# Kernel tuning notes

Measured on AMD Instinct MI355X. Metric: run time of the kernel, lower is better.

Reference implementation:

```python
import jax, jax.numpy as jnp
import numpy as np

N, T, E, H, V = 32768, 20, 50, 50, 200
PAD = 0

def setup_inputs() -> dict:
    key = jax.random.key(0)
    ks = jax.random.split(key, 11)
    s = 1.0 / np.sqrt(H)  # torch LSTM init scale
    return {
        "char_indices": jax.random.randint(ks[0], (N, T), 0, V, dtype=jnp.int32),
        "word_lengths": jax.random.randint(ks[1], (N,), 0, T + 1, dtype=jnp.int32),
        "emb": jax.random.normal(ks[2], (V, E), jnp.float32) * 0.1,
        "W_ih_f": jax.random.normal(ks[3], (4 * H, E), jnp.float32) * s,
        "W_hh_f": jax.random.normal(ks[4], (4 * H, H), jnp.float32) * s,
        "b_ih_f": jax.random.normal(ks[5], (4 * H,), jnp.float32) * s,
        "b_hh_f": jax.random.normal(ks[6], (4 * H,), jnp.float32) * s,
        "W_ih_b": jax.random.normal(ks[7], (4 * H, E), jnp.float32) * s,
        "W_hh_b": jax.random.normal(ks[8], (4 * H, H), jnp.float32) * s,
        "b_ih_b": jax.random.normal(ks[9], (4 * H,), jnp.float32) * s,
        "b_hh_b": jax.random.normal(ks[10], (4 * H,), jnp.float32) * s,
    }

def _run_dir(x, lengths, W_ih, W_hh, b_ih, b_hh, reverse):
    # x: [N,T,E]; returns final hidden state [N,H] at the word's true boundary.
    n = x.shape[0]
    xg = jnp.einsum('nte,ge->ntg', x, W_ih) + b_ih + b_hh  # [N,T,4H]
    def step(carry, t):
        h, c = carry
        g = xg[:, t] + h @ W_hh.T  # [N,4H]
        i, f, gg, o = jnp.split(g, 4, axis=-1)
        c_new = jax.nn.sigmoid(f) * c + jax.nn.sigmoid(i) * jnp.tanh(gg)
        h_new = jax.nn.sigmoid(o) * jnp.tanh(c_new)
        valid = (t < lengths)[:, None]  # only update inside the word
        return (jnp.where(valid, h_new, h), jnp.where(valid, c_new, c)), None
    ts = jnp.arange(T - 1, -1, -1) if reverse else jnp.arange(T)
    z = jnp.zeros((n, W_hh.shape[1]), x.dtype)
    (h, _), _ = jax.lax.scan(step, (z, z), ts)
    return h

def reference(char_indices, word_lengths, emb, W_ih_f, W_hh_f, b_ih_f, b_hh_f,
              W_ih_b, W_hh_b, b_ih_b, b_hh_b):
    emb = emb.at[PAD].set(0.0)  # padding_idx row is zero
    x = emb[char_indices]  # [N,T,E]
    h_f = _run_dir(x, word_lengths, W_ih_f, W_hh_f, b_ih_f, b_hh_f, reverse=False)
    h_b = _run_dir(x, word_lengths, W_ih_b, W_hh_b, b_ih_b, b_hh_b, reverse=True)
    return jnp.concatenate([h_f, h_b], axis=-1)  # [N, 2H]
```

## Files before the change

### kernel.cpp

```cpp
#include <hip/hip_runtime.h>


#define TT    20
#define HH    50
#define VV    200
#define TILES 13
#define GSTR  212
#define GSH   (VV * GSTR)
#define WSH   (TILES * 16 * 64)
#define NW    32768
#define NB_G  50
#define NB_W  104
#define NB_H  128
#define NBLK  1024

#define N2LOG2E (-1.4426950408889634f)
#define P2LOG2E 2.8853900817779268f

typedef __attribute__((ext_vector_type(8))) short bf16x8;
typedef __attribute__((ext_vector_type(4))) float f32x4;

__device__ __forceinline__ float frcp(float x) { return __builtin_amdgcn_rcpf(x); }
#if __has_builtin(__builtin_amdgcn_exp2f)
__device__ __forceinline__ float fexp2(float x) { return __builtin_amdgcn_exp2f(x); }
#else
__device__ __forceinline__ float fexp2(float x) { return exp2f(x); }
#endif

__device__ __forceinline__ short f2bf(float x) {
    unsigned b = __builtin_bit_cast(unsigned, x);
    unsigned r = (b + 0x7FFFu + ((b >> 16) & 1u)) >> 16;
    return (short)r;
}
__device__ __forceinline__ float bfhi(unsigned w) {
    return __builtin_bit_cast(float, w & 0xFFFF0000u);
}
__device__ __forceinline__ float bflo(unsigned w) {
    return __builtin_bit_cast(float, w << 16);
}

__global__ void k_prep(const float* __restrict__ emb,
                       const float* __restrict__ Wih_f, const float* __restrict__ bih_f,
                       const float* __restrict__ bhh_f,
                       const float* __restrict__ Wih_b, const float* __restrict__ bih_b,
                       const float* __restrict__ bhh_b,
                       const float* __restrict__ Whh_f, const float* __restrict__ Whh_b,
                       const int* __restrict__ lens,
                       short* __restrict__ Gimg, short* __restrict__ Wimg,
                       int* __restrict__ cnt) {
    int blk = blockIdx.x;
    int tid = threadIdx.x;
    __shared__ float Wl[4 * HH * HH];
    __shared__ float bs[4 * HH];

    if (blk < NB_G) {
        int d = blk / 25;
        int vbase = (blk % 25) * 8;
        const float* Wih = d ? Wih_b : Wih_f;
        const float* bih = d ? bih_b : bih_f;
        const float* bhh = d ? bhh_b : bhh_f;
        for (int i = tid; i < 4 * HH * HH; i += 256) {
            int r = i / HH;
            float sc = (r / HH == 2) ? P2LOG2E : N2LOG2E;
            Wl[i] = Wih[i] * sc;
        }
        if (tid < 4 * HH) {
            float sc = (tid / HH == 2) ? P2LOG2E : N2LOG2E;
            bs[tid] = (bih[tid] + bhh[tid]) * sc;
        }
        __syncthreads();
        int r = tid;
        if (r < 4 * HH) {
            int g = r / HH, u = r % HH;
            #pragma unroll
            for (int vv = 0; vv < 8; ++vv) {
                int v = vbase + vv;
                float s = bs[r];
                if (v != 0) {
                    #pragma unroll 10
                    for (int e = 0; e < HH; ++e)
                        s = fmaf(emb[v * HH + e], Wl[r * HH + e], s);
                }
                Gimg[d * GSH + v * GSTR + u * 4 + g] = f2bf(s);
            }
        } else {
            for (int k = r - 4 * HH; k < 8 * 12; k += 56) {
                int v = vbase + k / 12;
                Gimg[d * GSH + v * GSTR + 4 * HH + (k % 12)] = 0;
            }
        }
    } else if (blk < NB_G + NB_W) {
        int idx = (blk - NB_G) * 256 + tid;
        if (idx >= 2 * WSH) return;
        int d = idx / WSH;
        int e = idx % WSH;
        int t = e >> 10, m = (e >> 6) & 15, k = e & 63;
        int u = 4 * t + (m >> 2), g = m & 3;
        const float* Whh = d ? Whh_b : Whh_f;
        float sc = (g == 2) ? P2LOG2E : N2LOG2E;
        float val = (k < HH && u < HH) ? Whh[(g * HH + u) * HH + k] * sc : 0.0f;
        int ksw = (k & 7) | (((k >> 3) ^ (m & 7)) << 3);
        Wimg[d * WSH + (e & ~63) + ksw] = f2bf(val);
    } else {
        int hb = blk - NB_G - NB_W;
        __shared__ int hcnt[21];
        if (tid < 21) hcnt[tid] = 0;
        __syncthreads();
        atomicAdd(&hcnt[lens[hb * 256 + tid]], 1);
        __syncthreads();
        if (tid < 21) cnt[hb * 21 + tid] = hcnt[tid];
    }
}

__global__ void k_scat(const int* __restrict__ lens, const int* __restrict__ cnt,
                       int* __restrict__ perm) {
    __shared__ int lcnt[NB_H * 21];
    __shared__ int part[8][21];
    __shared__ int tot[21];
    __shared__ int cur[21];
    int b = blockIdx.x, t = threadIdx.x;
    for (int i = t; i < NB_H * 21; i += 256) lcnt[i] = cnt[i];
    __syncthreads();
    if (t < 168) {
        int L = t % 21, c = t / 21;
        int s = 0;
        for (int bb = c * 16; bb < c * 16 + 16; ++bb) s += lcnt[bb * 21 + L];
        part[c][L] = s;
    }
    __syncthreads();
    if (t < 21) {
        int a = 0;
        #pragma unroll
        for (int c = 0; c < 8; ++c) a += part[c][t];
        tot[t] = a;
    }
    __syncthreads();
    if (t < 21) {
        int a = 0;
        for (int L2 = 20; L2 > t; --L2) a += tot[L2];
        for (int bb = 0; bb < b; ++bb) a += lcnt[bb * 21 + t];
        cur[t] = a;
    }
    __syncthreads();
    int i = b * 256 + t;
    int pos = atomicAdd(&cur[lens[i]], 1);
    perm[pos] = i;
}

__launch_bounds__(256, 1)
__global__ void k_lstm(const int* __restrict__ chars, const int* __restrict__ lens,
                       const int* __restrict__ perm,
                       const short* __restrict__ Gimg, const short* __restrict__ Wimg,
                       float* __restrict__ out) {
    __shared__ __align__(16) short Wa[WSH];
    __shared__ __align__(16) short hs[4][1024];
    __shared__ unsigned short cs[4 * 16 * TT];

    int gb   = blockIdx.x;
    int d    = gb & 1;
    int g4   = gb >> 1;
    int slot0 = g4 * 64;
    int tid  = threadIdx.x;
    int lane = tid & 63;
    int wv   = __builtin_amdgcn_readfirstlane(tid >> 6);
    int quad = lane >> 4;
    int n    = lane & 15;
    int x7   = n & 7;

    {
        const int4* src = (const int4*)(Wimg + d * WSH);
        int4* dst = (int4*)Wa;
        for (int i = tid; i < WSH / 8; i += 256) dst[i] = src[i];
    }
    {
        int4 z = {0, 0, 0, 0};
        int4* hz = (int4*)&hs[0][0];
        hz[tid] = z;
        hz[tid + 256] = z;
    }
    for (int i = tid; i < 64 * TT; i += 256) {
        int w = perm[slot0 + i / TT];
        cs[i] = (unsigned short)(chars[w * TT + i % TT] * GSTR);
    }
    __syncthreads();

    int slotbase = slot0 + wv * 16;
    int word = perm[slotbase + n];
    int L = lens[word];
    int mL = L;
    #pragma unroll
    for (int off = 8; off; off >>= 1) {
        int t2 = __shfl_xor(mL, off);
        mL = mL > t2 ? mL : t2;
    }
    mL = __builtin_amdgcn_readfirstlane(mL);

    int pa0 = quad ^ x7;
    int pa1 = (quad + 4) ^ x7;

    const bf16x8* ap = (const bf16x8*)Wa;
    short* hw = hs[wv];
    const unsigned short* cw = cs + wv * 16 * TT + n * TT;
    const short* Gq = Gimg + d * GSH + quad * 4;

    float cst[TILES], hf[TILES];
    #pragma unroll
    for (int t = 0; t < TILES; ++t) { cst[t] = 0.0f; hf[t] = 0.0f; }

    int vcur = cw[(d && L > 0) ? (L - 1) : 0];

    #pragma unroll 1
    for (int s = 0; s < mL; ++s) {
        bool valid = s < L;

        bf16x8 B0 = *(const bf16x8*)(hw + n * 64 + pa0 * 8);
        bf16x8 B1 = *(const bf16x8*)(hw + n * 64 + pa1 * 8);

        int sn = s + 1;
        int pn = (sn < L) ? (d ? (L - 1 - sn) : sn) : 0;
        int vnxt = cw[pn];

        const int2* gp = (const int2*)(Gq + vcur);

        f32x4 acc[TILES];
        #pragma unroll
        for (int tt = 0; tt < TILES; ++tt) {
            int2 gw = gp[tt * 4];
            f32x4 a;
            a[0] = bflo((unsigned)gw.x);
            a[1] = bfhi((unsigned)gw.x);
            a[2] = bflo((unsigned)gw.y);
            a[3] = bfhi((unsigned)gw.y);
            bf16x8 A0 = ap[(tt * 16 + n) * 8 + pa0];
            bf16x8 A1 = ap[(tt * 16 + n) * 8 + pa1];
            a = __builtin_amdgcn_mfma_f32_16x16x32_bf16(A0, B0, a, 0, 0, 0);
            a = __builtin_amdgcn_mfma_f32_16x16x32_bf16(A1, B1, a, 0, 0, 0);
            acc[tt] = a;
        }
        #pragma unroll
        for (int tt = 0; tt < TILES; ++tt) {
            float ig = frcp(1.0f + fexp2(acc[tt][0]));
            float fg = frcp(1.0f + fexp2(acc[tt][1]));
            float tg = 1.0f - 2.0f * frcp(1.0f + fexp2(acc[tt][2]));
            float og = frcp(1.0f + fexp2(acc[tt][3]));
            float cn = fg * cst[tt] + ig * tg;
            float hn = og * (1.0f - 2.0f * frcp(1.0f + fexp2(cn * P2LOG2E)));
            int uu = 4 * tt + quad;
            bool upd = valid && (uu < HH);
            cst[tt] = upd ? cn : cst[tt];
            hf[tt]  = upd ? hn : hf[tt];
            if (upd) {
                int hidx = n * 64 + (((tt >> 1) ^ x7) << 3) + (tt & 1) * 4 + quad;
                hw[hidx] = f2bf(hn);
            }
        }
        vcur = vnxt;
    }

    float* orow = out + (size_t)word * (2 * HH) + d * HH;
    #pragma unroll
    for (int tt = 0; tt < TILES; ++tt) {
        int uu = 4 * tt + quad;
        if (uu < HH) orow[uu] = hf[tt];
    }
}

extern "C" void kernel_launch(void* const* d_in, const int* in_sizes, int n_in,
                              void* d_out, int out_size, void* d_ws, size_t ws_size,
                              hipStream_t stream) {
    const int*   chars = (const int*)d_in[0];
    const int*   lens  = (const int*)d_in[1];
    const float* emb   = (const float*)d_in[2];
    const float* Wih_f = (const float*)d_in[3];
    const float* Whh_f = (const float*)d_in[4];
    const float* bih_f = (const float*)d_in[5];
    const float* bhh_f = (const float*)d_in[6];
    const float* Wih_b = (const float*)d_in[7];
    const float* Whh_b = (const float*)d_in[8];
    const float* bih_b = (const float*)d_in[9];
    const float* bhh_b = (const float*)d_in[10];
    float* out = (float*)d_out;

    short* Gimg = (short*)d_ws;
    short* Wimg = Gimg + 2 * GSH;
    int*   cnt  = (int*)(Wimg + 2 * WSH);
    int*   perm = cnt + NB_H * 21;

    k_prep<<<NB_G + NB_W + NB_H, 256, 0, stream>>>(emb, Wih_f, bih_f, bhh_f,
                                                   Wih_b, bih_b, bhh_b,
                                                   Whh_f, Whh_b, lens,
                                                   Gimg, Wimg, cnt);
    k_scat<<<NB_H, 256, 0, stream>>>(lens, cnt, perm);
    k_lstm<<<NBLK, 256, 0, stream>>>(chars, lens, perm, Gimg, Wimg, out);
}
```

Baseline: 179.0 us.

## Process two length-balanced word groups per wave and prefetch gate rows

Halves the block count so each wave runs two passes, pairing a group from the long-word end of the length-sorted permutation with one from the short end to balance work across blocks. It also amortises the per-block weight copy into shared memory over twice as many words. The next step's input-gate row is now software-prefetched into registers during the MFMA phase instead of being loaded at the start of each step. In exchange the kernel holds more live registers and runs two serial passes per wave, which gives fewer waves in flight to hide latency.

```diff
diff --git a/kernel.cpp b/kernel.cpp
--- a/kernel.cpp
+++ b/kernel.cpp
@@ -12,7 +12,7 @@
 #define NB_G  50
 #define NB_W  104
 #define NB_H  128
-#define NBLK  1024
+#define NBLK  512
 
 #define N2LOG2E (-1.4426950408889634f)
 #define P2LOG2E 2.8853900817779268f
@@ -154,12 +154,11 @@
                        float* __restrict__ out) {
     __shared__ __align__(16) short Wa[WSH];
     __shared__ __align__(16) short hs[4][1024];
-    __shared__ unsigned short cs[4 * 16 * TT];
-
-    int gb   = blockIdx.x;
-    int d    = gb & 1;
-    int g4   = gb >> 1;
-    int slot0 = g4 * 64;
+    __shared__ unsigned short cs[4 * 2 * 16 * TT];
+
+    int b    = blockIdx.x;
+    int d    = b & 1;
+    int gbase = (b >> 1) * 4;
     int tid  = threadIdx.x;
     int lane = tid & 63;
     int wv   = __builtin_amdgcn_readfirstlane(tid >> 6);
@@ -172,96 +171,114 @@
         int4* dst = (int4*)Wa;
         for (int i = tid; i < WSH / 8; i += 256) dst[i] = src[i];
     }
-    {
-        int4 z = {0, 0, 0, 0};
-        int4* hz = (int4*)&hs[0][0];
-        hz[tid] = z;
-        hz[tid + 256] = z;
-    }
-    for (int i = tid; i < 64 * TT; i += 256) {
-        int w = perm[slot0 + i / TT];
-        cs[i] = (unsigned short)(chars[w * TT + i % TT] * GSTR);
-    }
-    __syncthreads();
-
-    int slotbase = slot0 + wv * 16;
-    int word = perm[slotbase + n];
-    int L = lens[word];
-    int mL = L;
-    #pragma unroll
-    for (int off = 8; off; off >>= 1) {
-        int t2 = __shfl_xor(mL, off);
-        mL = mL > t2 ? mL : t2;
-    }
-    mL = __builtin_amdgcn_readfirstlane(mL);
+    for (int i = tid; i < 4 * 2 * 16 * TT; i += 256) {
+        int w = i / 640;
+        int p = (i % 640) / 320;
+        int j = i % 320;
+        int g1 = gbase + w;
+        int g = p ? (2047 - g1) : g1;
+        int word = perm[g * 16 + j / TT];
+        cs[i] = (unsigned short)(chars[word * TT + j % TT] * GSTR);
+    }
+    __syncthreads();
 
     int pa0 = quad ^ x7;
     int pa1 = (quad + 4) ^ x7;
 
     const bf16x8* ap = (const bf16x8*)Wa;
     short* hw = hs[wv];
-    const unsigned short* cw = cs + wv * 16 * TT + n * TT;
     const short* Gq = Gimg + d * GSH + quad * 4;
-
-    float cst[TILES], hf[TILES];
-    #pragma unroll
-    for (int t = 0; t < TILES; ++t) { cst[t] = 0.0f; hf[t] = 0.0f; }
-
-    int vcur = cw[(d && L > 0) ? (L - 1) : 0];
+    int g1 = gbase + wv;
 
     #pragma unroll 1
-    for (int s = 0; s < mL; ++s) {
-        bool valid = s < L;
-
-        bf16x8 B0 = *(const bf16x8*)(hw + n * 64 + pa0 * 8);
-        bf16x8 B1 = *(const bf16x8*)(hw + n * 64 + pa1 * 8);
-
-        int sn = s + 1;
-        int pn = (sn < L) ? (d ? (L - 1 - sn) : sn) : 0;
-        int vnxt = cw[pn];
-
-        const int2* gp = (const int2*)(Gq + vcur);
-
-        f32x4 acc[TILES];
+    for (int pass = 0; pass < 2; ++pass) {
+        int g = pass ? (2047 - g1) : g1;
+        int word = perm[g * 16 + n];
+        int L = lens[word];
+        int mL = L;
+        #pragma unroll
+        for (int off = 8; off; off >>= 1) {
+            int t2 = __shfl_xor(mL, off);
+            mL = mL > t2 ? mL : t2;
+        }
+        mL = __builtin_amdgcn_readfirstlane(mL);
+
+        {
+            int4 z = {0, 0, 0, 0};
+            int4* hz = (int4*)hw;
+            hz[lane * 2] = z;
+            hz[lane * 2 + 1] = z;
+        }
+
+        const unsigned short* cw = cs + wv * 640 + pass * 320 + n * TT;
+        float cst[TILES], hf[TILES];
+        #pragma unroll
+        for (int t = 0; t < TILES; ++t) { cst[t] = 0.0f; hf[t] = 0.0f; }
+
+        int vcur = cw[(d && L > 0) ? (L - 1) : 0];
+        int2 gv[TILES];
+        {
+            const int2* gp = (const int2*)(Gq + vcur);
+            #pragma unroll
+            for (int tt = 0; tt < TILES; ++tt) gv[tt] = gp[tt * 4];
+        }
+
+        #pragma unroll 1
+        for (int s = 0; s < mL; ++s) {
+            bool valid = s < L;
+
+            bf16x8 B0 = *(const bf16x8*)(hw + n * 64 + pa0 * 8);
+            bf16x8 B1 = *(const bf16x8*)(hw + n * 64 + pa1 * 8);
+
+            int sn = s + 1;
+            int pn = (sn < L) ? (d ? (L - 1 - sn) : sn) : 0;
+            int vnxt = cw[pn];
+
+            f32x4 acc[TILES];
+            #pragma unroll
+            for (int tt = 0; tt < TILES; ++tt) {
+                int2 gw = gv[tt];
+                f32x4 a;
+                a[0] = bflo((unsigned)gw.x);
+                a[1] = bfhi((unsigned)gw.x);
+                a[2] = bflo((unsigned)gw.y);
+                a[3] = bfhi((unsigned)gw.y);
+                bf16x8 A0 = ap[(tt * 16 + n) * 8 + pa0];
+                bf16x8 A1 = ap[(tt * 16 + n) * 8 + pa1];
+                a = __builtin_amdgcn_mfma_f32_16x16x32_bf16(A0, B0, a, 0, 0, 0);
+                a = __builtin_amdgcn_mfma_f32_16x16x32_bf16(A1, B1, a, 0, 0, 0);
+                acc[tt] = a;
+            }
+            {
+                const int2* gp = (const int2*)(Gq + vnxt);
+                #pragma unroll
+                for (int tt = 0; tt < TILES; ++tt) gv[tt] = gp[tt * 4];
+            }
+            #pragma unroll
+            for (int tt = 0; tt < TILES; ++tt) {
+                float ig = frcp(1.0f + fexp2(acc[tt][0]));
+                float fg = frcp(1.0f + fexp2(acc[tt][1]));
+                float tg = 1.0f - 2.0f * frcp(1.0f + fexp2(acc[tt][2]));
+                float og = frcp(1.0f + fexp2(acc[tt][3]));
+                float cn = fg * cst[tt] + ig * tg;
+                float hn = og * (1.0f - 2.0f * frcp(1.0f + fexp2(cn * P2LOG2E)));
+                int uu = 4 * tt + quad;
+                bool upd = valid && (uu < HH);
+                cst[tt] = upd ? cn : cst[tt];
+                hf[tt]  = upd ? hn : hf[tt];
+                if (upd) {
+                    int hidx = n * 64 + (((tt >> 1) ^ x7) << 3) + (tt & 1) * 4 + quad;
+                    hw[hidx] = f2bf(hn);
+                }
+            }
+        }
+
+        float* orow = out + (size_t)word * (2 * HH) + d * HH;
         #pragma unroll
         for (int tt = 0; tt < TILES; ++tt) {
-            int2 gw = gp[tt * 4];
-            f32x4 a;
-            a[0] = bflo((unsigned)gw.x);
-            a[1] = bfhi((unsigned)gw.x);
-            a[2] = bflo((unsigned)gw.y);
-            a[3] = bfhi((unsigned)gw.y);
-            bf16x8 A0 = ap[(tt * 16 + n) * 8 + pa0];
-            bf16x8 A1 = ap[(tt * 16 + n) * 8 + pa1];
-            a = __builtin_amdgcn_mfma_f32_16x16x32_bf16(A0, B0, a, 0, 0, 0);
-            a = __builtin_amdgcn_mfma_f32_16x16x32_bf16(A1, B1, a, 0, 0, 0);
-            acc[tt] = a;
-        }
-        #pragma unroll
-        for (int tt = 0; tt < TILES; ++tt) {
-            float ig = frcp(1.0f + fexp2(acc[tt][0]));
-            float fg = frcp(1.0f + fexp2(acc[tt][1]));
-            float tg = 1.0f - 2.0f * frcp(1.0f + fexp2(acc[tt][2]));
-            float og = frcp(1.0f + fexp2(acc[tt][3]));
-            float cn = fg * cst[tt] + ig * tg;
-            float hn = og * (1.0f - 2.0f * frcp(1.0f + fexp2(cn * P2LOG2E)));
             int uu = 4 * tt + quad;
-            bool upd = valid && (uu < HH);
-            cst[tt] = upd ? cn : cst[tt];
-            hf[tt]  = upd ? hn : hf[tt];
-            if (upd) {
-                int hidx = n * 64 + (((tt >> 1) ^ x7) << 3) + (tt & 1) * 4 + quad;
-                hw[hidx] = f2bf(hn);
-            }
-        }
-        vcur = vnxt;
-    }
-
-    float* orow = out + (size_t)word * (2 * HH) + d * HH;
-    #pragma unroll
-    for (int tt = 0; tt < TILES; ++tt) {
-        int uu = 4 * tt + quad;
-        if (uu < HH) orow[uu] = hf[tt];
+            if (uu < HH) orow[uu] = hf[tt];
+        }
     }
 }
 
```

New measurement: 192.2 us. +7.4%, slower.
